# Performance work log

Measured on AMD Instinct MI355X. Metric: run time of the kernel, lower is better.

Reference implementation:

```python
import jax, jax.numpy as jnp
import numpy as np

B, L, D = 4, 2048, 768
H, K = 12, 9
IPG = D // H  # in-channels per group = head_size = 64
PAD = (K - 1) // 2


def setup_inputs() -> dict:
    key = jax.random.key(0)
    ks = jax.random.split(key, 8)
    s = lambda k, shape, scale: jax.random.normal(k, shape, dtype=jnp.float32) * scale
    return {
        "query": s(ks[0], (B, L, D), 1.0),
        "dw_w": s(ks[1], (D, 1, K), 0.1),          # depthwise Conv1d weight, no bias
        "pw_w": s(ks[2], (H, IPG, IPG), 0.05),     # grouped 1x1 conv [head, out_pg, in_pg]
        "pw_b": s(ks[3], (D,), 0.02),
        "ak_w": s(ks[4], (H, K, IPG), 0.05),       # conv_attn_kernel grouped 1x1 [head, K, in_pg]
        "ak_b": s(ks[5], (H * K,), 0.02),
        "pt_w": s(ks[6], (D, D), 0.02),            # conv_attn_point Linear weight [out, in]
        "pt_b": s(ks[7], (D,), 0.02),
    }


def _sdconv(query, dw_w, pw_w, pw_b, ak_w, ak_b, pt_w, pt_b):
    b, l, d = query.shape
    # SeparableConv1d: depthwise conv (groups=D, kernel K, padding PAD, no bias)
    x = query.transpose(0, 2, 1)  # [B, D, L]
    dw = jax.lax.conv_general_dilated(
        x, dw_w, window_strides=(1,), padding=[(PAD, PAD)],
        feature_group_count=d, dimension_numbers=("NCH", "OIH", "NCH"))  # [B, D, L]
    # grouped pointwise conv (groups=H, kernel 1)
    dwg = dw.reshape(b, H, IPG, l)
    pw = jnp.einsum("bhil,hoi->bhol", dwg, pw_w).reshape(b, d, l) + pw_b[None, :, None]
    key_conv_attn = pw.transpose(0, 2, 1)  # [B, L, D]
    # stride == 1 path: elementwise gate with query
    conv_attn = key_conv_attn * query  # [B, L, D]
    # conv_attn_kernel: grouped 1x1 conv D -> H*K (per head: IPG -> K)
    ca = conv_attn.reshape(b, l, H, IPG)
    kern = jnp.einsum("blhi,hki->blhk", ca, ak_w) + ak_b.reshape(H, K)  # [B, L, H, K]
    w = jax.nn.softmax(kern, axis=-1)  # softmax over kernel positions
    # conv_attn_point linear on value (= query here)
    v = query @ pt_w.T + pt_b  # [B, L, D]
    # unfold: local windows of size K around each position
    vp = jnp.pad(v, ((0, 0), (PAD, PAD), (0, 0)))
    idx = jnp.arange(l)[:, None] + jnp.arange(K)[None, :]  # [L, K]
    win = vp[:, idx]  # [B, L, K, D]
    winh = win.reshape(b, l, K, H, IPG)
    out = jnp.einsum("blkhd,blhk->blhd", winh, w).reshape(b, l, d)
    return out


def reference(query, dw_w, pw_w, pw_b, ak_w, ak_b, pt_w, pt_b):
    return _sdconv(query, dw_w, pw_w, pw_b, ak_w, ak_b, pt_w, pt_b)
```

## Files before the change

### kernel.cpp

```cpp
#include <hip/hip_runtime.h>
#include <math.h>

#define NB 4
#define NL 2048
#define ND 768
#define NH 12
#define NK 9
#define NIPG 64
#define NPAD 4
#define MT 112

typedef __attribute__((ext_vector_type(8))) short s16x8;
typedef __attribute__((ext_vector_type(4))) float f32x4;

__device__ __forceinline__ unsigned short f2bf(float f) {
  unsigned int u = __float_as_uint(f);
  unsigned int r = (u + 0x7FFFu + ((u >> 16) & 1u)) >> 16;
  return (unsigned short)r;
}
__device__ __forceinline__ float bf2f(unsigned short s) {
  return __uint_as_float(((unsigned int)s) << 16);
}
__device__ __forceinline__ void gload16(const void* g, void* l) {
  __builtin_amdgcn_global_load_lds((const __attribute__((address_space(1))) void*)g,
                                   (__attribute__((address_space(3))) void*)l,
                                   16, 0, 0);
}

__global__ __launch_bounds__(256) void prep(const float* __restrict__ pt_w,
                                            const float* __restrict__ pw_w,
                                            const float* __restrict__ ak_w,
                                            unsigned short* __restrict__ ptb,
                                            unsigned short* __restrict__ pwb,
                                            unsigned short* __restrict__ akp) {
  const int t = blockIdx.x * 256 + threadIdx.x;
  if (t < ND * ND / 4) {
    float4 f = ((const float4*)pt_w)[t];
    ushort4 o; o.x = f2bf(f.x); o.y = f2bf(f.y); o.z = f2bf(f.z); o.w = f2bf(f.w);
    ((ushort4*)ptb)[t] = o;
  }
  if (t < NH * NIPG * NIPG / 4) {
    float4 f = ((const float4*)pw_w)[t];
    ushort4 o; o.x = f2bf(f.x); o.y = f2bf(f.y); o.z = f2bf(f.z); o.w = f2bf(f.w);
    ((ushort4*)pwb)[t] = o;
  }
  if (t < NH * 16 * NIPG) {
    const int h = t >> 10;
    const int r = t & 1023;
    const int k = r >> 6;
    const int i = r & 63;
    akp[t] = (k < NK) ? f2bf(ak_w[((size_t)h * NK + k) * NIPG + i]) : (unsigned short)0;
  }
}

__global__ __launch_bounds__(256) void attn_w(const float* __restrict__ q,
                                              const float* __restrict__ dw_w,
                                              const unsigned short* __restrict__ pwb,
                                              const float* __restrict__ pw_b,
                                              const unsigned short* __restrict__ akp,
                                              const float* __restrict__ ak_b,
                                              float* __restrict__ wout,
                                              unsigned short* __restrict__ qb) {
  __shared__ unsigned short qs[72][68];
  __shared__ unsigned char ab[8192];
  const int l0 = blockIdx.x * 64;
  const int h  = blockIdx.y;
  const int b  = blockIdx.z;
  const int d0 = h * NIPG;
  const int t  = threadIdx.x;
  const int lane = t & 63;
  const int wv = t >> 6;

  {
    const int sl = t >> 4;
    const int sc = (t & 15) * 4;
    for (int r = sl; r < 72; r += 16) {
      const int l = l0 - NPAD + r;
      ushort4 ub = make_ushort4(0, 0, 0, 0);
      if (l >= 0 && l < NL) {
        float4 val = *(const float4*)&q[((size_t)(b * NL + l)) * ND + d0 + sc];
        ub.x = f2bf(val.x); ub.y = f2bf(val.y); ub.z = f2bf(val.z); ub.w = f2bf(val.w);
        if (r >= NPAD && r < NPAD + 64)
          *(ushort4*)&qb[((size_t)(b * NL + l)) * ND + d0 + sc] = ub;
      }
      *(ushort4*)&qs[r][sc] = ub;
    }
  }
  float dwk[NK];
#pragma unroll
  for (int k = 0; k < NK; ++k) dwk[k] = dw_w[(size_t)(d0 + lane) * NK + k];
  __syncthreads();

  const int lset = wv * 16;
  {
    float win9[NK];
#pragma unroll
    for (int k = 0; k < NK; ++k) win9[k] = bf2f(qs[lset + k][lane]);
#pragma unroll
    for (int l2 = 0; l2 < 16; ++l2) {
      const int l = lset + l2;
      float s = 0.f;
#pragma unroll
      for (int k = 0; k < NK; ++k) s = fmaf(win9[k], dwk[k], s);
      const int byte = ((l * 64 + lane) * 2) ^ ((l & 7) << 4);
      *(unsigned short*)&ab[byte] = f2bf(s);
      if (l2 < 15) {
#pragma unroll
        for (int k = 0; k < NK - 1; ++k) win9[k] = win9[k + 1];
        win9[NK - 1] = bf2f(qs[lset + l2 + NK][lane]);
      }
    }
  }
  __syncthreads();

  const int fr = lane & 15;
  const int fq = lane >> 4;

  s16x8 av0, av1;
  {
    const int row = lset + fr;
    const int b0 = ((row * 64 + fq * 8) * 2)      ^ ((row & 7) << 4);
    const int b1 = ((row * 64 + 32 + fq * 8) * 2) ^ ((row & 7) << 4);
    av0 = *(const s16x8*)&ab[b0];
    av1 = *(const s16x8*)&ab[b1];
  }
  const unsigned short* pwh = pwb + (size_t)h * NIPG * NIPG;
  f32x4 accp[4];
#pragma unroll
  for (int n = 0; n < 4; ++n) {
    accp[n] = (f32x4){0.f, 0.f, 0.f, 0.f};
    const int o = n * 16 + fr;
    s16x8 bv0 = *(const s16x8*)&pwh[o * 64 + fq * 8];
    s16x8 bv1 = *(const s16x8*)&pwh[o * 64 + 32 + fq * 8];
    accp[n] = __builtin_amdgcn_mfma_f32_16x16x32_bf16(av0, bv0, accp[n], 0, 0, 0);
    accp[n] = __builtin_amdgcn_mfma_f32_16x16x32_bf16(av1, bv1, accp[n], 0, 0, 0);
  }
  __syncthreads();

#pragma unroll
  for (int n = 0; n < 4; ++n) {
    const int o = n * 16 + fr;
    const float pb = pw_b[d0 + o];
#pragma unroll
    for (int j = 0; j < 4; ++j) {
      const int row = lset + fq * 4 + j;
      const float ca = (accp[n][j] + pb) * bf2f(qs[row + NPAD][o]);
      const int byte = ((row * 64 + o) * 2) ^ ((row & 7) << 4);
      *(unsigned short*)&ab[byte] = f2bf(ca);
    }
  }
  __syncthreads();

  f32x4 acck = (f32x4){0.f, 0.f, 0.f, 0.f};
  {
    const int row = lset + fr;
    const int b0 = ((row * 64 + fq * 8) * 2)      ^ ((row & 7) << 4);
    const int b1 = ((row * 64 + 32 + fq * 8) * 2) ^ ((row & 7) << 4);
    s16x8 a0 = *(const s16x8*)&ab[b0];
    s16x8 a1 = *(const s16x8*)&ab[b1];
    const unsigned short* akh = akp + (size_t)h * 16 * NIPG;
    s16x8 b0v = *(const s16x8*)&akh[fr * 64 + fq * 8];
    s16x8 b1v = *(const s16x8*)&akh[fr * 64 + 32 + fq * 8];
    acck = __builtin_amdgcn_mfma_f32_16x16x32_bf16(a0, b0v, acck, 0, 0, 0);
    acck = __builtin_amdgcn_mfma_f32_16x16x32_bf16(a1, b1v, acck, 0, 0, 0);
  }

  const bool kvalid = fr < NK;
  const float akbv = kvalid ? ak_b[h * NK + fr] : 0.f;
#pragma unroll
  for (int j = 0; j < 4; ++j) {
    float val = acck[j] + akbv;
    float mv = kvalid ? val : -3.4e38f;
#pragma unroll
    for (int mm = 1; mm < 16; mm <<= 1) mv = fmaxf(mv, __shfl_xor(mv, mm));
    const float e = kvalid ? __expf(val - mv) : 0.f;
    float ssum = e;
#pragma unroll
    for (int mm = 1; mm < 16; mm <<= 1) ssum += __shfl_xor(ssum, mm);
    if (kvalid) {
      const int row = l0 + lset + fq * 4 + j;
      wout[(((size_t)(b * NL + row)) * NH + h) * NK + fr] = e / ssum;
    }
  }
}

__global__ __launch_bounds__(256) void gemm_conv(const unsigned short* __restrict__ qb,
                                                 const unsigned short* __restrict__ ptb,
                                                 const float* __restrict__ bias,
                                                 const float* __restrict__ w,
                                                 float* __restrict__ out) {
  __shared__ unsigned char lds[24576];
  const int t = threadIdx.x;
  const long mo = (long)blockIdx.x * MT;
  const int n0 = blockIdx.y * 64;
  const int lane = t & 63;
  const int wv = t >> 6;
  const int fr = lane & 15;
  const int fq = lane >> 4;

  const int soff = t * 16;
  const int sr = soff >> 6;
  const int scb = soff & 63;
  const unsigned char* gA0 = (const unsigned char*)qb + (mo - 8 + sr) * (long)(ND * 2) + scb;
  const unsigned char* gA1 = gA0 + (long)64 * (ND * 2);
  const unsigned char* gB  = (const unsigned char*)ptb + (size_t)(n0 + sr) * (ND * 2) + scb;

  int aoff[2], boff[4];
#pragma unroll
  for (int m = 0; m < 2; ++m)
    aoff[m] = ((wv * 32 + m * 16 + fr) * 32 + fq * 8) * 2;
#pragma unroll
  for (int n = 0; n < 4; ++n)
    boff[n] = 8192 + ((n * 16 + fr) * 32 + fq * 8) * 2;

#define STAGE(kt, buf)                                             \
  do {                                                             \
    const long kb_ = (long)(kt) * 64;                              \
    unsigned char* base_ = &lds[(buf) * 12288];                    \
    gload16(gA0 + kb_, base_ + soff);                              \
    gload16(gA1 + kb_, base_ + 4096 + soff);                       \
    if (soff < 4096) gload16(gB + kb_, base_ + 8192 + soff);       \
  } while (0)

  f32x4 acc[2][4] = {};
  STAGE(0, 0);
  __syncthreads();
  for (int kt = 0; kt < ND / 32; ++kt) {
    const int cur = kt & 1;
    if (kt + 1 < ND / 32) STAGE(kt + 1, cur ^ 1);
    const unsigned char* bb = &lds[cur * 12288];
    s16x8 av[2], bv[4];
#pragma unroll
    for (int m = 0; m < 2; ++m) av[m] = *(const s16x8*)&bb[aoff[m]];
#pragma unroll
    for (int n = 0; n < 4; ++n) bv[n] = *(const s16x8*)&bb[boff[n]];
#pragma unroll
    for (int m = 0; m < 2; ++m)
#pragma unroll
      for (int n = 0; n < 4; ++n)
        acc[m][n] = __builtin_amdgcn_mfma_f32_16x16x32_bf16(av[m], bv[n], acc[m][n], 0, 0, 0);
    __syncthreads();
  }
#undef STAGE

  unsigned short* vt = (unsigned short*)lds;
#pragma unroll
  for (int m = 0; m < 2; ++m) {
#pragma unroll
    for (int n = 0; n < 4; ++n) {
      const int rb = wv * 32 + m * 16 + fq * 4;
      const int cc = n * 16 + fr;
      const float bbv = bias[n0 + cc];
#pragma unroll
      for (int j = 0; j < 4; ++j)
        vt[(rb + j) * 68 + cc] = f2bf(acc[m][n][j] + bbv);
    }
  }
  __syncthreads();

  const int cq = (t & 15) * 4;
  const int r0 = 8 + (t >> 4) * 7;
  const int h = n0 >> 6;
  float4 win[NK];
#pragma unroll
  for (int k = 0; k < NK; ++k) {
    ushort4 u = *(const ushort4*)&vt[(r0 - 4 + k) * 68 + cq];
    win[k] = make_float4(bf2f(u.x), bf2f(u.y), bf2f(u.z), bf2f(u.w));
  }
#pragma unroll
  for (int i = 0; i < 7; ++i) {
    const int r = r0 + i;
    const long g = mo + r - 8;
    if (g < (long)NB * NL) {
      const int l = (int)(g & (NL - 1));
      const float* wp = &w[((size_t)g * NH + h) * NK];
      float4 a = make_float4(0.f, 0.f, 0.f, 0.f);
#pragma unroll
      for (int k = 0; k < NK; ++k) {
        const int lk = l + k - NPAD;
        if (lk >= 0 && lk < NL) {
          const float wk = wp[k];
          a.x = fmaf(wk, win[k].x, a.x);
          a.y = fmaf(wk, win[k].y, a.y);
          a.z = fmaf(wk, win[k].z, a.z);
          a.w = fmaf(wk, win[k].w, a.w);
        }
      }
      *(float4*)&out[(size_t)g * ND + n0 + cq] = a;
    }
    if (i < 6) {
#pragma unroll
      for (int k = 0; k < NK - 1; ++k) win[k] = win[k + 1];
      ushort4 u = *(const ushort4*)&vt[(r + 5) * 68 + cq];
      win[NK - 1] = make_float4(bf2f(u.x), bf2f(u.y), bf2f(u.z), bf2f(u.w));
    }
  }
}

extern "C" void kernel_launch(void* const* d_in, const int* in_sizes, int n_in,
                              void* d_out, int out_size, void* d_ws, size_t ws_size,
                              hipStream_t stream) {
  const float* query = (const float*)d_in[0];
  const float* dw_w  = (const float*)d_in[1];
  const float* pw_w  = (const float*)d_in[2];
  const float* pw_b  = (const float*)d_in[3];
  const float* ak_w  = (const float*)d_in[4];
  const float* ak_b  = (const float*)d_in[5];
  const float* pt_w  = (const float*)d_in[6];
  const float* pt_b  = (const float*)d_in[7];
  float* out = (float*)d_out;

  float* w = (float*)d_ws;
  unsigned short* qb  = (unsigned short*)(w + (size_t)NB * NL * NH * NK);
  unsigned short* ptb = qb + (size_t)NB * NL * ND;
  unsigned short* pwb = ptb + (size_t)ND * ND;
  unsigned short* akp = pwb + (size_t)NH * NIPG * NIPG;

  prep<<<ND * ND / 4 / 256, 256, 0, stream>>>(pt_w, pw_w, ak_w, ptb, pwb, akp);

  dim3 g2(NL / 64, NH, NB);
  attn_w<<<g2, 256, 0, stream>>>(query, dw_w, pwb, pw_b, akp, ak_b, w, qb);

  dim3 g3((NB * NL + MT - 1) / MT, ND / 64, 1);
  gemm_conv<<<g3, 256, 0, stream>>>(qb, ptb, pt_b, w, out);
}
```

Measured before the change: 141.1 us.

## Load GEMM fragments directly from global into registers, drop LDS staging and barriers

The projection GEMM no longer stages A/B tiles through LDS with global_load_lds and per-iteration barriers. Each wave now loads its MFMA fragments straight from global memory into registers, double-buffered across k-steps. In attn_w, the pointwise and attention-kernel weight fragments are hoisted to the kernel start, and two __syncthreads are removed. This trades the LDS traffic and barrier stalls for redundant, less coalesced global/L2 reads, since fragments are no longer shared between waves. The removed barriers are only safe because each wave reads back its own 16 rows of LDS.

```diff
diff --git a/kernel.cpp b/kernel.cpp
--- a/kernel.cpp
+++ b/kernel.cpp
@@ -20,11 +20,6 @@
 }
 __device__ __forceinline__ float bf2f(unsigned short s) {
   return __uint_as_float(((unsigned int)s) << 16);
-}
-__device__ __forceinline__ void gload16(const void* g, void* l) {
-  __builtin_amdgcn_global_load_lds((const __attribute__((address_space(1))) void*)g,
-                                   (__attribute__((address_space(3))) void*)l,
-                                   16, 0, 0);
 }
 
 __global__ __launch_bounds__(256) void prep(const float* __restrict__ pt_w,
@@ -70,6 +65,23 @@
   const int t  = threadIdx.x;
   const int lane = t & 63;
   const int wv = t >> 6;
+  const int fr = lane & 15;
+  const int fq = lane >> 4;
+
+  const unsigned short* pwh = pwb + (size_t)h * NIPG * NIPG;
+  const unsigned short* akh = akp + (size_t)h * 16 * NIPG;
+  s16x8 pv0[4], pv1[4];
+#pragma unroll
+  for (int n = 0; n < 4; ++n) {
+    const int o = n * 16 + fr;
+    pv0[n] = *(const s16x8*)&pwh[o * 64 + fq * 8];
+    pv1[n] = *(const s16x8*)&pwh[o * 64 + 32 + fq * 8];
+  }
+  s16x8 ak0 = *(const s16x8*)&akh[fr * 64 + fq * 8];
+  s16x8 ak1 = *(const s16x8*)&akh[fr * 64 + 32 + fq * 8];
+  float dwk[NK];
+#pragma unroll
+  for (int k = 0; k < NK; ++k) dwk[k] = dw_w[(size_t)(d0 + lane) * NK + k];
 
   {
     const int sl = t >> 4;
@@ -86,9 +98,6 @@
       *(ushort4*)&qs[r][sc] = ub;
     }
   }
-  float dwk[NK];
-#pragma unroll
-  for (int k = 0; k < NK; ++k) dwk[k] = dw_w[(size_t)(d0 + lane) * NK + k];
   __syncthreads();
 
   const int lset = wv * 16;
@@ -111,10 +120,6 @@
       }
     }
   }
-  __syncthreads();
-
-  const int fr = lane & 15;
-  const int fq = lane >> 4;
 
   s16x8 av0, av1;
   {
@@ -124,18 +129,13 @@
     av0 = *(const s16x8*)&ab[b0];
     av1 = *(const s16x8*)&ab[b1];
   }
-  const unsigned short* pwh = pwb + (size_t)h * NIPG * NIPG;
   f32x4 accp[4];
 #pragma unroll
   for (int n = 0; n < 4; ++n) {
     accp[n] = (f32x4){0.f, 0.f, 0.f, 0.f};
-    const int o = n * 16 + fr;
-    s16x8 bv0 = *(const s16x8*)&pwh[o * 64 + fq * 8];
-    s16x8 bv1 = *(const s16x8*)&pwh[o * 64 + 32 + fq * 8];
-    accp[n] = __builtin_amdgcn_mfma_f32_16x16x32_bf16(av0, bv0, accp[n], 0, 0, 0);
-    accp[n] = __builtin_amdgcn_mfma_f32_16x16x32_bf16(av1, bv1, accp[n], 0, 0, 0);
-  }
-  __syncthreads();
+    accp[n] = __builtin_amdgcn_mfma_f32_16x16x32_bf16(av0, pv0[n], accp[n], 0, 0, 0);
+    accp[n] = __builtin_amdgcn_mfma_f32_16x16x32_bf16(av1, pv1[n], accp[n], 0, 0, 0);
+  }
 
 #pragma unroll
   for (int n = 0; n < 4; ++n) {
@@ -149,7 +149,6 @@
       *(unsigned short*)&ab[byte] = f2bf(ca);
     }
   }
-  __syncthreads();
 
   f32x4 acck = (f32x4){0.f, 0.f, 0.f, 0.f};
   {
@@ -158,11 +157,8 @@
     const int b1 = ((row * 64 + 32 + fq * 8) * 2) ^ ((row & 7) << 4);
     s16x8 a0 = *(const s16x8*)&ab[b0];
     s16x8 a1 = *(const s16x8*)&ab[b1];
-    const unsigned short* akh = akp + (size_t)h * 16 * NIPG;
-    s16x8 b0v = *(const s16x8*)&akh[fr * 64 + fq * 8];
-    s16x8 b1v = *(const s16x8*)&akh[fr * 64 + 32 + fq * 8];
-    acck = __builtin_amdgcn_mfma_f32_16x16x32_bf16(a0, b0v, acck, 0, 0, 0);
-    acck = __builtin_amdgcn_mfma_f32_16x16x32_bf16(a1, b1v, acck, 0, 0, 0);
+    acck = __builtin_amdgcn_mfma_f32_16x16x32_bf16(a0, ak0, acck, 0, 0, 0);
+    acck = __builtin_amdgcn_mfma_f32_16x16x32_bf16(a1, ak1, acck, 0, 0, 0);
   }
 
   const bool kvalid = fr < NK;
@@ -189,7 +185,7 @@
                                                  const float* __restrict__ bias,
                                                  const float* __restrict__ w,
                                                  float* __restrict__ out) {
-  __shared__ unsigned char lds[24576];
+  __shared__ unsigned short vt[128 * 68];
   const int t = threadIdx.x;
   const long mo = (long)blockIdx.x * MT;
   const int n0 = blockIdx.y * 64;
@@ -198,52 +194,43 @@
   const int fr = lane & 15;
   const int fq = lane >> 4;
 
-  const int soff = t * 16;
-  const int sr = soff >> 6;
-  const int scb = soff & 63;
-  const unsigned char* gA0 = (const unsigned char*)qb + (mo - 8 + sr) * (long)(ND * 2) + scb;
-  const unsigned char* gA1 = gA0 + (long)64 * (ND * 2);
-  const unsigned char* gB  = (const unsigned char*)ptb + (size_t)(n0 + sr) * (ND * 2) + scb;
-
-  int aoff[2], boff[4];
-#pragma unroll
-  for (int m = 0; m < 2; ++m)
-    aoff[m] = ((wv * 32 + m * 16 + fr) * 32 + fq * 8) * 2;
-#pragma unroll
-  for (int n = 0; n < 4; ++n)
-    boff[n] = 8192 + ((n * 16 + fr) * 32 + fq * 8) * 2;
-
-#define STAGE(kt, buf)                                             \
-  do {                                                             \
-    const long kb_ = (long)(kt) * 64;                              \
-    unsigned char* base_ = &lds[(buf) * 12288];                    \
-    gload16(gA0 + kb_, base_ + soff);                              \
-    gload16(gA1 + kb_, base_ + 4096 + soff);                       \
-    if (soff < 4096) gload16(gB + kb_, base_ + 8192 + soff);       \
+  const unsigned short* pa = qb + (mo - 8 + wv * 32 + fr) * (long)ND + fq * 8;
+  const unsigned short* pb = ptb + (size_t)(n0 + fr) * ND + fq * 8;
+
+  s16x8 af[2][2], bf[2][4];
+  f32x4 acc[2][4] = {};
+
+#define LOADK(buf, kt)                                                  \
+  do {                                                                  \
+    const long ko_ = (long)(kt) * 32;                                   \
+    _Pragma("unroll")                                                   \
+    for (int m = 0; m < 2; ++m)                                         \
+      af[buf][m] = *(const s16x8*)(pa + (long)m * 16 * ND + ko_);       \
+    _Pragma("unroll")                                                   \
+    for (int n = 0; n < 4; ++n)                                         \
+      bf[buf][n] = *(const s16x8*)(pb + (long)n * 16 * ND + ko_);       \
   } while (0)
 
-  f32x4 acc[2][4] = {};
-  STAGE(0, 0);
-  __syncthreads();
-  for (int kt = 0; kt < ND / 32; ++kt) {
-    const int cur = kt & 1;
-    if (kt + 1 < ND / 32) STAGE(kt + 1, cur ^ 1);
-    const unsigned char* bb = &lds[cur * 12288];
-    s16x8 av[2], bv[4];
-#pragma unroll
-    for (int m = 0; m < 2; ++m) av[m] = *(const s16x8*)&bb[aoff[m]];
-#pragma unroll
-    for (int n = 0; n < 4; ++n) bv[n] = *(const s16x8*)&bb[boff[n]];
-#pragma unroll
-    for (int m = 0; m < 2; ++m)
-#pragma unroll
-      for (int n = 0; n < 4; ++n)
-        acc[m][n] = __builtin_amdgcn_mfma_f32_16x16x32_bf16(av[m], bv[n], acc[m][n], 0, 0, 0);
-    __syncthreads();
-  }
-#undef STAGE
-
-  unsigned short* vt = (unsigned short*)lds;
+#define MMSET(buf)                                                      \
+  do {                                                                  \
+    _Pragma("unroll")                                                   \
+    for (int m = 0; m < 2; ++m)                                         \
+      _Pragma("unroll")                                                 \
+      for (int n = 0; n < 4; ++n)                                       \
+        acc[m][n] = __builtin_amdgcn_mfma_f32_16x16x32_bf16(            \
+            af[buf][m], bf[buf][n], acc[m][n], 0, 0, 0);                \
+  } while (0)
+
+  LOADK(0, 0);
+  for (int kt = 0; kt < ND / 32; kt += 2) {
+    LOADK(1, kt + 1);
+    MMSET(0);
+    if (kt + 2 < ND / 32) LOADK(0, kt + 2);
+    MMSET(1);
+  }
+#undef LOADK
+#undef MMSET
+
 #pragma unroll
   for (int m = 0; m < 2; ++m) {
 #pragma unroll
```

New measurement: 187.5 us. +32.8%, slower.

## Merge V GEMM and attention-weight kernel into one launch, split out window conv

Applied to the files above, without the earlier changes.

The query-to-bf16 conversion now happens in the prep kernel over a grid-stride loop. The projection GEMM and the attention-weight computation run as two block roles inside one launch, so they execute concurrently. GEMM blocks use an XCD-aware tile mapping, no longer need halo rows, and write V to global memory in bf16. A separate lightweight kernel then applies the softmax-weighted 9-tap window over V. This removes the redundant halo GEMM work and the serialization between the attention and GEMM stages, at the cost of one extra global round trip for V and an additional launch.

```diff
diff --git a/kernel.cpp b/kernel.cpp
--- a/kernel.cpp
+++ b/kernel.cpp
@@ -8,7 +8,8 @@
 #define NK 9
 #define NIPG 64
 #define NPAD 4
-#define MT 112
+#define LT 16
+#define NGEMM 768
 
 typedef __attribute__((ext_vector_type(8))) short s16x8;
 typedef __attribute__((ext_vector_type(4))) float f32x4;
@@ -27,13 +28,20 @@
                                    16, 0, 0);
 }
 
-__global__ __launch_bounds__(256) void prep(const float* __restrict__ pt_w,
+__global__ __launch_bounds__(256) void prep(const float* __restrict__ q,
+                                            const float* __restrict__ pt_w,
                                             const float* __restrict__ pw_w,
                                             const float* __restrict__ ak_w,
+                                            unsigned short* __restrict__ qb,
                                             unsigned short* __restrict__ ptb,
                                             unsigned short* __restrict__ pwb,
                                             unsigned short* __restrict__ akp) {
   const int t = blockIdx.x * 256 + threadIdx.x;
+  for (int i = t; i < NB * NL * ND / 4; i += gridDim.x * 256) {
+    float4 f = ((const float4*)q)[i];
+    ushort4 o; o.x = f2bf(f.x); o.y = f2bf(f.y); o.z = f2bf(f.z); o.w = f2bf(f.w);
+    ((ushort4*)qb)[i] = o;
+  }
   if (t < ND * ND / 4) {
     float4 f = ((const float4*)pt_w)[t];
     ushort4 o; o.x = f2bf(f.x); o.y = f2bf(f.y); o.z = f2bf(f.z); o.w = f2bf(f.w);
@@ -53,246 +61,249 @@
   }
 }
 
-__global__ __launch_bounds__(256) void attn_w(const float* __restrict__ q,
-                                              const float* __restrict__ dw_w,
-                                              const unsigned short* __restrict__ pwb,
-                                              const float* __restrict__ pw_b,
-                                              const unsigned short* __restrict__ akp,
-                                              const float* __restrict__ ak_b,
-                                              float* __restrict__ wout,
-                                              unsigned short* __restrict__ qb) {
-  __shared__ unsigned short qs[72][68];
-  __shared__ unsigned char ab[8192];
-  const int l0 = blockIdx.x * 64;
-  const int h  = blockIdx.y;
-  const int b  = blockIdx.z;
-  const int d0 = h * NIPG;
-  const int t  = threadIdx.x;
-  const int lane = t & 63;
-  const int wv = t >> 6;
-
-  {
-    const int sl = t >> 4;
-    const int sc = (t & 15) * 4;
-    for (int r = sl; r < 72; r += 16) {
-      const int l = l0 - NPAD + r;
-      ushort4 ub = make_ushort4(0, 0, 0, 0);
-      if (l >= 0 && l < NL) {
-        float4 val = *(const float4*)&q[((size_t)(b * NL + l)) * ND + d0 + sc];
-        ub.x = f2bf(val.x); ub.y = f2bf(val.y); ub.z = f2bf(val.z); ub.w = f2bf(val.w);
-        if (r >= NPAD && r < NPAD + 64)
-          *(ushort4*)&qb[((size_t)(b * NL + l)) * ND + d0 + sc] = ub;
-      }
-      *(ushort4*)&qs[r][sc] = ub;
-    }
-  }
-  float dwk[NK];
-#pragma unroll
-  for (int k = 0; k < NK; ++k) dwk[k] = dw_w[(size_t)(d0 + lane) * NK + k];
-  __syncthreads();
-
-  const int lset = wv * 16;
-  {
-    float win9[NK];
-#pragma unroll
-    for (int k = 0; k < NK; ++k) win9[k] = bf2f(qs[lset + k][lane]);
-#pragma unroll
-    for (int l2 = 0; l2 < 16; ++l2) {
-      const int l = lset + l2;
-      float s = 0.f;
-#pragma unroll
-      for (int k = 0; k < NK; ++k) s = fmaf(win9[k], dwk[k], s);
-      const int byte = ((l * 64 + lane) * 2) ^ ((l & 7) << 4);
-      *(unsigned short*)&ab[byte] = f2bf(s);
-      if (l2 < 15) {
-#pragma unroll
-        for (int k = 0; k < NK - 1; ++k) win9[k] = win9[k + 1];
-        win9[NK - 1] = bf2f(qs[lset + l2 + NK][lane]);
-      }
-    }
-  }
-  __syncthreads();
-
-  const int fr = lane & 15;
-  const int fq = lane >> 4;
-
-  s16x8 av0, av1;
-  {
-    const int row = lset + fr;
-    const int b0 = ((row * 64 + fq * 8) * 2)      ^ ((row & 7) << 4);
-    const int b1 = ((row * 64 + 32 + fq * 8) * 2) ^ ((row & 7) << 4);
-    av0 = *(const s16x8*)&ab[b0];
-    av1 = *(const s16x8*)&ab[b1];
-  }
-  const unsigned short* pwh = pwb + (size_t)h * NIPG * NIPG;
-  f32x4 accp[4];
-#pragma unroll
-  for (int n = 0; n < 4; ++n) {
-    accp[n] = (f32x4){0.f, 0.f, 0.f, 0.f};
-    const int o = n * 16 + fr;
-    s16x8 bv0 = *(const s16x8*)&pwh[o * 64 + fq * 8];
-    s16x8 bv1 = *(const s16x8*)&pwh[o * 64 + 32 + fq * 8];
-    accp[n] = __builtin_amdgcn_mfma_f32_16x16x32_bf16(av0, bv0, accp[n], 0, 0, 0);
-    accp[n] = __builtin_amdgcn_mfma_f32_16x16x32_bf16(av1, bv1, accp[n], 0, 0, 0);
-  }
-  __syncthreads();
-
-#pragma unroll
-  for (int n = 0; n < 4; ++n) {
-    const int o = n * 16 + fr;
-    const float pb = pw_b[d0 + o];
-#pragma unroll
-    for (int j = 0; j < 4; ++j) {
-      const int row = lset + fq * 4 + j;
-      const float ca = (accp[n][j] + pb) * bf2f(qs[row + NPAD][o]);
-      const int byte = ((row * 64 + o) * 2) ^ ((row & 7) << 4);
-      *(unsigned short*)&ab[byte] = f2bf(ca);
-    }
-  }
-  __syncthreads();
-
-  f32x4 acck = (f32x4){0.f, 0.f, 0.f, 0.f};
-  {
-    const int row = lset + fr;
-    const int b0 = ((row * 64 + fq * 8) * 2)      ^ ((row & 7) << 4);
-    const int b1 = ((row * 64 + 32 + fq * 8) * 2) ^ ((row & 7) << 4);
-    s16x8 a0 = *(const s16x8*)&ab[b0];
-    s16x8 a1 = *(const s16x8*)&ab[b1];
-    const unsigned short* akh = akp + (size_t)h * 16 * NIPG;
-    s16x8 b0v = *(const s16x8*)&akh[fr * 64 + fq * 8];
-    s16x8 b1v = *(const s16x8*)&akh[fr * 64 + 32 + fq * 8];
-    acck = __builtin_amdgcn_mfma_f32_16x16x32_bf16(a0, b0v, acck, 0, 0, 0);
-    acck = __builtin_amdgcn_mfma_f32_16x16x32_bf16(a1, b1v, acck, 0, 0, 0);
-  }
-
-  const bool kvalid = fr < NK;
-  const float akbv = kvalid ? ak_b[h * NK + fr] : 0.f;
-#pragma unroll
-  for (int j = 0; j < 4; ++j) {
-    float val = acck[j] + akbv;
-    float mv = kvalid ? val : -3.4e38f;
-#pragma unroll
-    for (int mm = 1; mm < 16; mm <<= 1) mv = fmaxf(mv, __shfl_xor(mv, mm));
-    const float e = kvalid ? __expf(val - mv) : 0.f;
-    float ssum = e;
-#pragma unroll
-    for (int mm = 1; mm < 16; mm <<= 1) ssum += __shfl_xor(ssum, mm);
-    if (kvalid) {
-      const int row = l0 + lset + fq * 4 + j;
-      wout[(((size_t)(b * NL + row)) * NH + h) * NK + fr] = e / ssum;
-    }
-  }
-}
-
-__global__ __launch_bounds__(256) void gemm_conv(const unsigned short* __restrict__ qb,
-                                                 const unsigned short* __restrict__ ptb,
-                                                 const float* __restrict__ bias,
-                                                 const float* __restrict__ w,
-                                                 float* __restrict__ out) {
-  __shared__ unsigned char lds[24576];
+__global__ __launch_bounds__(256) void fused(const unsigned short* __restrict__ qb,
+                                             const unsigned short* __restrict__ ptb,
+                                             const float* __restrict__ bias,
+                                             unsigned short* __restrict__ v,
+                                             const float* __restrict__ dw_w,
+                                             const unsigned short* __restrict__ pwb,
+                                             const float* __restrict__ pw_b,
+                                             const unsigned short* __restrict__ akp,
+                                             const float* __restrict__ ak_b,
+                                             float* __restrict__ wout) {
+  __shared__ unsigned char smem[24576];
   const int t = threadIdx.x;
-  const long mo = (long)blockIdx.x * MT;
-  const int n0 = blockIdx.y * 64;
   const int lane = t & 63;
   const int wv = t >> 6;
   const int fr = lane & 15;
   const int fq = lane >> 4;
 
-  const int soff = t * 16;
-  const int sr = soff >> 6;
-  const int scb = soff & 63;
-  const unsigned char* gA0 = (const unsigned char*)qb + (mo - 8 + sr) * (long)(ND * 2) + scb;
-  const unsigned char* gA1 = gA0 + (long)64 * (ND * 2);
-  const unsigned char* gB  = (const unsigned char*)ptb + (size_t)(n0 + sr) * (ND * 2) + scb;
-
-  int aoff[2], boff[4];
-#pragma unroll
-  for (int m = 0; m < 2; ++m)
-    aoff[m] = ((wv * 32 + m * 16 + fr) * 32 + fq * 8) * 2;
-#pragma unroll
-  for (int n = 0; n < 4; ++n)
-    boff[n] = 8192 + ((n * 16 + fr) * 32 + fq * 8) * 2;
-
-#define STAGE(kt, buf)                                             \
-  do {                                                             \
-    const long kb_ = (long)(kt) * 64;                              \
-    unsigned char* base_ = &lds[(buf) * 12288];                    \
-    gload16(gA0 + kb_, base_ + soff);                              \
-    gload16(gA1 + kb_, base_ + 4096 + soff);                       \
-    if (soff < 4096) gload16(gB + kb_, base_ + 8192 + soff);       \
-  } while (0)
-
-  f32x4 acc[2][4] = {};
-  STAGE(0, 0);
-  __syncthreads();
-  for (int kt = 0; kt < ND / 32; ++kt) {
-    const int cur = kt & 1;
-    if (kt + 1 < ND / 32) STAGE(kt + 1, cur ^ 1);
-    const unsigned char* bb = &lds[cur * 12288];
-    s16x8 av[2], bv[4];
-#pragma unroll
-    for (int m = 0; m < 2; ++m) av[m] = *(const s16x8*)&bb[aoff[m]];
-#pragma unroll
-    for (int n = 0; n < 4; ++n) bv[n] = *(const s16x8*)&bb[boff[n]];
+  if (blockIdx.x < NGEMM) {
+    const int g = blockIdx.x;
+    const int xcd = g & 7;
+    const int j = g >> 3;
+    const long mo = (long)(xcd * 8 + j / 12) * 128;
+    const int n0 = (j % 12) * 64;
+
+    const int soff = t * 16;
+    const int sr = soff >> 6;
+    const int scb = soff & 63;
+    const unsigned char* gA0 = (const unsigned char*)qb + (mo + sr) * 1536L + scb;
+    const unsigned char* gA1 = gA0 + 64L * 1536;
+    const unsigned char* gB  = (const unsigned char*)ptb + (size_t)(n0 + sr) * 1536 + scb;
+
+    int aoff[2], boff[4];
 #pragma unroll
     for (int m = 0; m < 2; ++m)
-#pragma unroll
-      for (int n = 0; n < 4; ++n)
-        acc[m][n] = __builtin_amdgcn_mfma_f32_16x16x32_bf16(av[m], bv[n], acc[m][n], 0, 0, 0);
+      aoff[m] = ((wv * 32 + m * 16 + fr) * 32 + fq * 8) * 2;
+#pragma unroll
+    for (int n = 0; n < 4; ++n)
+      boff[n] = 8192 + ((n * 16 + fr) * 32 + fq * 8) * 2;
+
+#define STAGE(kt_, buf_)                                           \
+    do {                                                           \
+      const long kb_ = (long)(kt_) * 64;                           \
+      unsigned char* base_ = &smem[(buf_) * 12288];                \
+      gload16(gA0 + kb_, base_ + soff);                            \
+      gload16(gA1 + kb_, base_ + 4096 + soff);                     \
+      gload16(gB + kb_, base_ + 8192 + soff);                      \
+    } while (0)
+
+    f32x4 acc[2][4] = {};
+    STAGE(0, 0);
     __syncthreads();
-  }
+    for (int kt = 0; kt < ND / 32; ++kt) {
+      const int cur = kt & 1;
+      if (kt + 1 < ND / 32) STAGE(kt + 1, cur ^ 1);
+      const unsigned char* bb = &smem[cur * 12288];
+      s16x8 av[2], bv[4];
+#pragma unroll
+      for (int m = 0; m < 2; ++m) av[m] = *(const s16x8*)&bb[aoff[m]];
+#pragma unroll
+      for (int n = 0; n < 4; ++n) bv[n] = *(const s16x8*)&bb[boff[n]];
+#pragma unroll
+      for (int m = 0; m < 2; ++m)
+#pragma unroll
+        for (int n = 0; n < 4; ++n)
+          acc[m][n] = __builtin_amdgcn_mfma_f32_16x16x32_bf16(av[m], bv[n], acc[m][n], 0, 0, 0);
+      __syncthreads();
+    }
 #undef STAGE
 
-  unsigned short* vt = (unsigned short*)lds;
-#pragma unroll
-  for (int m = 0; m < 2; ++m) {
+#pragma unroll
+    for (int m = 0; m < 2; ++m) {
+#pragma unroll
+      for (int n = 0; n < 4; ++n) {
+        const long row = mo + wv * 32 + m * 16 + fq * 4;
+        const int col = n0 + n * 16 + fr;
+        const float bbv = bias[col];
+#pragma unroll
+        for (int jj = 0; jj < 4; ++jj)
+          v[(row + jj) * ND + col] = f2bf(acc[m][n][jj] + bbv);
+      }
+    }
+  } else {
+    const int a = blockIdx.x - NGEMM;
+    const int l0 = (a & 31) * 64;
+    const int h  = (a >> 5) % NH;
+    const int b  = a / (32 * NH);
+    const int d0 = h * NIPG;
+
+    unsigned short (*qs)[68] = (unsigned short(*)[68])smem;
+    unsigned char* ab = smem + 9792;
+
+    const unsigned short* pwh = pwb + (size_t)h * NIPG * NIPG;
+    const unsigned short* akh = akp + (size_t)h * 16 * NIPG;
+    s16x8 pv0[4], pv1[4];
 #pragma unroll
     for (int n = 0; n < 4; ++n) {
-      const int rb = wv * 32 + m * 16 + fq * 4;
-      const int cc = n * 16 + fr;
-      const float bbv = bias[n0 + cc];
-#pragma unroll
-      for (int j = 0; j < 4; ++j)
-        vt[(rb + j) * 68 + cc] = f2bf(acc[m][n][j] + bbv);
-    }
-  }
-  __syncthreads();
-
-  const int cq = (t & 15) * 4;
-  const int r0 = 8 + (t >> 4) * 7;
-  const int h = n0 >> 6;
+      const int o = n * 16 + fr;
+      pv0[n] = *(const s16x8*)&pwh[o * 64 + fq * 8];
+      pv1[n] = *(const s16x8*)&pwh[o * 64 + 32 + fq * 8];
+    }
+    s16x8 ak0 = *(const s16x8*)&akh[fr * 64 + fq * 8];
+    s16x8 ak1 = *(const s16x8*)&akh[fr * 64 + 32 + fq * 8];
+    float dwk[NK];
+#pragma unroll
+    for (int k = 0; k < NK; ++k) dwk[k] = dw_w[(size_t)(d0 + lane) * NK + k];
+
+    {
+      const int sl = t >> 4;
+      const int sc = (t & 15) * 4;
+      for (int r = sl; r < 72; r += 16) {
+        const int l = l0 - NPAD + r;
+        ushort4 ub = make_ushort4(0, 0, 0, 0);
+        if (l >= 0 && l < NL)
+          ub = *(const ushort4*)&qb[((size_t)(b * NL + l)) * ND + d0 + sc];
+        *(ushort4*)&qs[r][sc] = ub;
+      }
+    }
+    __syncthreads();
+
+    const int lset = wv * 16;
+    {
+      float win9[NK];
+#pragma unroll
+      for (int k = 0; k < NK; ++k) win9[k] = bf2f(qs[lset + k][lane]);
+#pragma unroll
+      for (int l2 = 0; l2 < 16; ++l2) {
+        const int l = lset + l2;
+        float s = 0.f;
+#pragma unroll
+        for (int k = 0; k < NK; ++k) s = fmaf(win9[k], dwk[k], s);
+        const int byte = ((l * 64 + lane) * 2) ^ ((l & 7) << 4);
+        *(unsigned short*)&ab[byte] = f2bf(s);
+        if (l2 < 15) {
+#pragma unroll
+          for (int k = 0; k < NK - 1; ++k) win9[k] = win9[k + 1];
+          win9[NK - 1] = bf2f(qs[lset + l2 + NK][lane]);
+        }
+      }
+    }
+
+    s16x8 av0, av1;
+    {
+      const int row = lset + fr;
+      const int b0 = ((row * 64 + fq * 8) * 2)      ^ ((row & 7) << 4);
+      const int b1 = ((row * 64 + 32 + fq * 8) * 2) ^ ((row & 7) << 4);
+      av0 = *(const s16x8*)&ab[b0];
+      av1 = *(const s16x8*)&ab[b1];
+    }
+    f32x4 accp[4];
+#pragma unroll
+    for (int n = 0; n < 4; ++n) {
+      accp[n] = (f32x4){0.f, 0.f, 0.f, 0.f};
+      accp[n] = __builtin_amdgcn_mfma_f32_16x16x32_bf16(av0, pv0[n], accp[n], 0, 0, 0);
+      accp[n] = __builtin_amdgcn_mfma_f32_16x16x32_bf16(av1, pv1[n], accp[n], 0, 0, 0);
+    }
+
+#pragma unroll
+    for (int n = 0; n < 4; ++n) {
+      const int o = n * 16 + fr;
+      const float pb = pw_b[d0 + o];
+#pragma unroll
+      for (int jj = 0; jj < 4; ++jj) {
+        const int row = lset + fq * 4 + jj;
+        const float ca = (accp[n][jj] + pb) * bf2f(qs[row + NPAD][o]);
+        const int byte = ((row * 64 + o) * 2) ^ ((row & 7) << 4);
+        *(unsigned short*)&ab[byte] = f2bf(ca);
+      }
+    }
+
+    f32x4 acck = (f32x4){0.f, 0.f, 0.f, 0.f};
+    {
+      const int row = lset + fr;
+      const int b0 = ((row * 64 + fq * 8) * 2)      ^ ((row & 7) << 4);
+      const int b1 = ((row * 64 + 32 + fq * 8) * 2) ^ ((row & 7) << 4);
+      s16x8 a0 = *(const s16x8*)&ab[b0];
+      s16x8 a1 = *(const s16x8*)&ab[b1];
+      acck = __builtin_amdgcn_mfma_f32_16x16x32_bf16(a0, ak0, acck, 0, 0, 0);
+      acck = __builtin_amdgcn_mfma_f32_16x16x32_bf16(a1, ak1, acck, 0, 0, 0);
+    }
+
+    const bool kvalid = fr < NK;
+    const float akbv = kvalid ? ak_b[h * NK + fr] : 0.f;
+#pragma unroll
+    for (int jj = 0; jj < 4; ++jj) {
+      float val = acck[jj] + akbv;
+      float mv = kvalid ? val : -3.4e38f;
+#pragma unroll
+      for (int mm = 1; mm < 16; mm <<= 1) mv = fmaxf(mv, __shfl_xor(mv, mm));
+      const float e = kvalid ? __expf(val - mv) : 0.f;
+      float ssum = e;
+#pragma unroll
+      for (int mm = 1; mm < 16; mm <<= 1) ssum += __shfl_xor(ssum, mm);
+      if (kvalid) {
+        const int row = l0 + lset + fq * 4 + jj;
+        wout[(((size_t)(b * NL + row)) * NH + h) * NK + fr] = e / ssum;
+      }
+    }
+  }
+}
+
+__global__ __launch_bounds__(192) void sdconv_out(const unsigned short* __restrict__ v,
+                                                  const float* __restrict__ w,
+                                                  float* __restrict__ out) {
+  const int b  = blockIdx.y;
+  const int l0 = blockIdx.x * LT;
+  const int t  = threadIdx.x;
+  const int d  = t * 4;
+  const int h  = t >> 4;
+  const size_t vbase = (size_t)b * NL * ND + d;
+
   float4 win[NK];
 #pragma unroll
   for (int k = 0; k < NK; ++k) {
-    ushort4 u = *(const ushort4*)&vt[(r0 - 4 + k) * 68 + cq];
-    win[k] = make_float4(bf2f(u.x), bf2f(u.y), bf2f(u.z), bf2f(u.w));
-  }
-#pragma unroll
-  for (int i = 0; i < 7; ++i) {
-    const int r = r0 + i;
-    const long g = mo + r - 8;
-    if (g < (long)NB * NL) {
-      const int l = (int)(g & (NL - 1));
-      const float* wp = &w[((size_t)g * NH + h) * NK];
-      float4 a = make_float4(0.f, 0.f, 0.f, 0.f);
-#pragma unroll
-      for (int k = 0; k < NK; ++k) {
-        const int lk = l + k - NPAD;
-        if (lk >= 0 && lk < NL) {
-          const float wk = wp[k];
-          a.x = fmaf(wk, win[k].x, a.x);
-          a.y = fmaf(wk, win[k].y, a.y);
-          a.z = fmaf(wk, win[k].z, a.z);
-          a.w = fmaf(wk, win[k].w, a.w);
-        }
-      }
-      *(float4*)&out[(size_t)g * ND + n0 + cq] = a;
-    }
-    if (i < 6) {
-#pragma unroll
-      for (int k = 0; k < NK - 1; ++k) win[k] = win[k + 1];
-      ushort4 u = *(const ushort4*)&vt[(r + 5) * 68 + cq];
+    const int r = l0 - NPAD + k;
+    if (r >= 0 && r < NL) {
+      ushort4 u = *(const ushort4*)&v[vbase + (size_t)r * ND];
+      win[k] = make_float4(bf2f(u.x), bf2f(u.y), bf2f(u.z), bf2f(u.w));
+    } else {
+      win[k] = make_float4(0.f, 0.f, 0.f, 0.f);
+    }
+  }
+#pragma unroll
+  for (int l2 = 0; l2 < LT; ++l2) {
+    const int l = l0 + l2;
+    const float* wp = &w[(((size_t)(b * NL + l)) * NH + h) * NK];
+    float4 acc = make_float4(0.f, 0.f, 0.f, 0.f);
+#pragma unroll
+    for (int k = 0; k < NK; ++k) {
+      const float wk = wp[k];
+      acc.x = fmaf(wk, win[k].x, acc.x);
+      acc.y = fmaf(wk, win[k].y, acc.y);
+      acc.z = fmaf(wk, win[k].z, acc.z);
+      acc.w = fmaf(wk, win[k].w, acc.w);
+    }
+    *(float4*)&out[(size_t)(b * NL + l) * ND + d] = acc;
+#pragma unroll
+    for (int k = 0; k < NK - 1; ++k) win[k] = win[k + 1];
+    const int rn = l + NPAD + 1;
+    if (rn < NL) {
+      ushort4 u = *(const ushort4*)&v[vbase + (size_t)rn * ND];
       win[NK - 1] = make_float4(bf2f(u.x), bf2f(u.y), bf2f(u.z), bf2f(u.w));
+    } else {
+      win[NK - 1] = make_float4(0.f, 0.f, 0.f, 0.f);
     }
   }
 }
@@ -315,12 +326,13 @@
   unsigned short* ptb = qb + (size_t)NB * NL * ND;
   unsigned short* pwb = ptb + (size_t)ND * ND;
   unsigned short* akp = pwb + (size_t)NH * NIPG * NIPG;
-
-  prep<<<ND * ND / 4 / 256, 256, 0, stream>>>(pt_w, pw_w, ak_w, ptb, pwb, akp);
-
-  dim3 g2(NL / 64, NH, NB);
-  attn_w<<<g2, 256, 0, stream>>>(query, dw_w, pwb, pw_b, akp, ak_b, w, qb);
-
-  dim3 g3((NB * NL + MT - 1) / MT, ND / 64, 1);
-  gemm_conv<<<g3, 256, 0, stream>>>(qb, ptb, pt_b, w, out);
-}
+  unsigned short* v   = akp + (size_t)NH * 16 * NIPG;
+
+  prep<<<2048, 256, 0, stream>>>(query, pt_w, pw_w, ak_w, qb, ptb, pwb, akp);
+
+  fused<<<NGEMM + 32 * NH * NB, 256, 0, stream>>>(qb, ptb, pt_b, v,
+                                                  dw_w, pwb, pw_b, akp, ak_b, w);
+
+  dim3 g3(NL / LT, NB, 1);
+  sdconv_out<<<g3, 192, 0, stream>>>(v, w, out);
+}
```

New measurement: 139.9 us. About the same (-0.9%).
